# Kernel optimization log

Measured on AMD Instinct MI355X. Metric: run time of the kernel, lower is better.

Reference implementation:

```python
import jax, jax.numpy as jnp
import numpy as np
import math

EMBED_DIM = 1024
N_HEAD = 16
HEAD_DIM = EMBED_DIM // N_HEAD


def setup_inputs() -> dict:
    key = jax.random.key(0)
    ks = jax.random.split(key, 9)
    B, T, C = 4, 2048, EMBED_DIM
    s = 1.0 / math.sqrt(C)
    return {
        "x": jax.random.normal(ks[0], (B, T, C), dtype=jnp.float32),
        "Wq": jax.random.normal(ks[1], (C, C), dtype=jnp.float32) * s,
        "bq": jnp.zeros((C,), dtype=jnp.float32),
        "Wk": jax.random.normal(ks[2], (C, C), dtype=jnp.float32) * s,
        "bk": jnp.zeros((C,), dtype=jnp.float32),
        "Wv": jax.random.normal(ks[3], (C, C), dtype=jnp.float32) * s,
        "bv": jnp.zeros((C,), dtype=jnp.float32),
        "Wp": jax.random.normal(ks[4], (C, C), dtype=jnp.float32) * s,
        "bp": jnp.zeros((C,), dtype=jnp.float32),
    }


def reference(x, Wq, bq, Wk, bk, Wv, bv, Wp, bp):
    B, T, C = x.shape
    H, D = N_HEAD, HEAD_DIM

    def heads(W, b):
        # [B,T,C] -> [B,H,T,D]
        return (x @ W.T + b).reshape(B, T, H, D).transpose(0, 2, 1, 3)

    q = heads(Wq, bq)
    k = heads(Wk, bk)
    v = heads(Wv, bv)

    att = jnp.einsum("bhtd,bhsd->bhts", q, k) * (1.0 / math.sqrt(D))
    causal = jnp.tril(jnp.ones((T, T), dtype=bool))
    att = jnp.where(causal[None, None], att, -jnp.inf)
    att = jax.nn.softmax(att, axis=-1)
    y = jnp.einsum("bhts,bhsd->bhtd", att, v)  # [B,H,T,D]
    y = y.transpose(0, 2, 1, 3).reshape(B, T, C)
    return y @ Wp.T + bp
```

## Files before the change

### kernel.cpp

```cpp
#include <hip/hip_runtime.h>
#include <hip/hip_bf16.h>
#include <cstdint>
#include <cstddef>

#define TQ 2048
#define CDIM 1024
#define NH 16
#define HD 64

typedef __attribute__((ext_vector_type(8))) short bf16x8;
typedef __attribute__((ext_vector_type(4))) float f32x4;
typedef __attribute__((ext_vector_type(16))) float f32x16;

__device__ __forceinline__ unsigned short f2bf(float f) {
  union { float f; unsigned u; } x; x.f = f;
  unsigned r = x.u + 0x7fffu + ((x.u >> 16) & 1u);
  return (unsigned short)(r >> 16);
}

__device__ __forceinline__ unsigned cvtpk(float lo, float hi) {
  unsigned r;
  asm("v_cvt_pk_bf16_f32 %0, %1, %2" : "=v"(r) : "v"(lo), "v"(hi));
  return r;
}

__device__ __forceinline__ void plswap(unsigned& x, unsigned& y) {
  asm("v_permlane32_swap_b32 %0, %1" : "+v"(x), "+v"(y));
}

__device__ __forceinline__ float exp2_fast(float x) {
  float r;
  asm("v_exp_f32 %0, %1" : "=v"(r) : "v"(x));
  return r;
}

__device__ __forceinline__ void gload_lds16(const void* g, void* l) {
  typedef __attribute__((address_space(1))) const void gv;
  typedef __attribute__((address_space(3))) void lv;
  __builtin_amdgcn_global_load_lds((gv*)g, (lv*)l, 16, 0, 0);
}

__global__ void cvt_bf16_kernel(const float* __restrict__ in,
                                unsigned short* __restrict__ out, int n) {
  int stride = gridDim.x * blockDim.x;
  for (int i = blockIdx.x * blockDim.x + threadIdx.x; i * 4 < n; i += stride) {
    float4 v = *(const float4*)(in + (size_t)i * 4);
    ushort4 o;
    o.x = f2bf(v.x); o.y = f2bf(v.y); o.z = f2bf(v.z); o.w = f2bf(v.w);
    *(ushort4*)(out + (size_t)i * 4) = o;
  }
}

__global__ void cvt4_kernel(const float* __restrict__ w0, const float* __restrict__ w1,
                            const float* __restrict__ w2, const float* __restrict__ w3,
                            unsigned short* __restrict__ out) {
  int i = blockIdx.x * blockDim.x + threadIdx.x;
  int which = i >> 18;
  const float* src = which == 0 ? w0 : which == 1 ? w1 : which == 2 ? w2 : w3;
  int off = (i & 262143) * 4;
  float4 v = *(const float4*)(src + off);
  ushort4 o;
  o.x = f2bf(v.x); o.y = f2bf(v.y); o.z = f2bf(v.z); o.w = f2bf(v.w);
  *(ushort4*)(out + (size_t)i * 4) = o;
}

template <int EPI>
__global__ __launch_bounds__(256) void gemm_bt_kernel(
    const unsigned short* __restrict__ A,
    const unsigned short* __restrict__ Bt,
    const float* __restrict__ b0, const float* __restrict__ b1,
    void* __restrict__ outp,
    int M, int N, int K) {
  __shared__ __align__(16) unsigned short As[128 * 64];
  __shared__ __align__(16) unsigned short Bs[128 * 64];

  const int nbm = M >> 7;
  const int nbn = N >> 7;
  const int nwg = nbm * nbn;
  int id = (int)blockIdx.x;
  const int cpx = nwg >> 3;
  id = (id & 7) * cpx + (id >> 3);
  const int tm = id % nbm;
  const int tn = id / nbm;

  const int tid = threadIdx.x;
  const int w = tid >> 6, lane = tid & 63;
  const int g = lane >> 4, c = lane & 15;
  const int wr = w >> 1, wc = w & 1;

  const unsigned short* Ab = A + (size_t)tm * 128 * K;
  const unsigned short* Bb = Bt + (size_t)tn * 128 * K;
  const int Kb = K * 2;

  f32x4 acc[4][4];
#pragma unroll
  for (int i = 0; i < 4; ++i)
#pragma unroll
    for (int j = 0; j < 4; ++j) acc[i][j] = (f32x4){0.f, 0.f, 0.f, 0.f};

  for (int kt = 0; kt < K; kt += 64) {
#pragma unroll
    for (int i = 0; i < 4; ++i) {
      const int seg = w * 4 + i;
      const int off = seg * 1024 + lane * 16;
      const int row = off >> 7;
      const int colB = off & 127;
      gload_lds16((const char*)Ab + (size_t)row * Kb + kt * 2 + colB,
                  (char*)As + seg * 1024);
      gload_lds16((const char*)Bb + (size_t)row * Kb + kt * 2 + colB,
                  (char*)Bs + seg * 1024);
    }
    __syncthreads();
#pragma unroll
    for (int ki = 0; ki < 2; ++ki) {
      bf16x8 af[4], bv[4];
#pragma unroll
      for (int mi = 0; mi < 4; ++mi)
        af[mi] = *(const bf16x8*)(As + (wr * 64 + mi * 16 + c) * 64 + ki * 32 + g * 8);
#pragma unroll
      for (int ni = 0; ni < 4; ++ni)
        bv[ni] = *(const bf16x8*)(Bs + (wc * 64 + ni * 16 + c) * 64 + ki * 32 + g * 8);
#pragma unroll
      for (int mi = 0; mi < 4; ++mi)
#pragma unroll
        for (int ni = 0; ni < 4; ++ni)
          acc[mi][ni] = __builtin_amdgcn_mfma_f32_16x16x32_bf16(
              af[mi], bv[ni], acc[mi][ni], 0, 0, 0);
    }
    __syncthreads();
  }

#pragma unroll
  for (int mi = 0; mi < 4; ++mi) {
#pragma unroll
    for (int ni = 0; ni < 4; ++ni) {
      const int n = tn * 128 + wc * 64 + ni * 16 + c;
#pragma unroll
      for (int e = 0; e < 4; ++e) {
        const int m = tm * 128 + wr * 64 + mi * 16 + g * 4 + e;
        float v = acc[mi][ni][e];
        if (EPI == 1) {
          v += b0[m];
          size_t idx = ((size_t)(n >> 11) * (NH * HD) + m) * TQ + (n & (TQ - 1));
          ((unsigned short*)outp)[idx] = f2bf(v);
        } else if (EPI == 2) {
          v += b0[n];
          ((float*)outp)[(size_t)m * N + n] = v;
        } else {
          unsigned short* O = (unsigned short*)outp;
          if (n < 1024) {
            v += b0[n];
            size_t idx = ((size_t)(m >> 11) * NH + (n >> 6)) * (TQ * HD) +
                         (size_t)(m & (TQ - 1)) * HD + (n & (HD - 1));
            O[idx] = f2bf(v);
          } else {
            int nn = n - 1024;
            v += b1[nn];
            size_t idx = 8388608 + ((size_t)(m >> 11) * NH + (nn >> 6)) * (TQ * HD) +
                         (size_t)(m & (TQ - 1)) * HD + (nn & (HD - 1));
            O[idx] = f2bf(v);
          }
        }
      }
    }
  }
}

__global__ __launch_bounds__(256) void attn_kernel(
    const unsigned short* __restrict__ Q,
    const unsigned short* __restrict__ K,
    const unsigned short* __restrict__ Vt,
    unsigned short* __restrict__ Y) {
  __shared__ __align__(16) unsigned short Ks[2][4096];
  __shared__ __align__(16) unsigned short Vs[2][4096];

  const int tid = (int)threadIdx.x;
  const int w = tid >> 6, lane = tid & 63;
  const int l31 = lane & 31, hi = lane >> 5;
  const int sx = (l31 & 7) << 4;
  const int bh = (int)blockIdx.y;
  const int b = bh >> 4, h = bh & 15;

  const unsigned short* Qb = Q + (size_t)bh * TQ * HD;
  const char* Kb = (const char*)(K + (size_t)bh * TQ * HD);
  const char* Vb = (const char*)(Vt + (size_t)bh * HD * TQ);

  auto stage = [&](int buf, int kt) {
#pragma unroll
    for (int i = 0; i < 2; ++i) {
      const int o = (tid << 4) + (i << 12);
      const int row = o >> 7;
      const int scol = (o & 127) ^ ((row & 7) << 4);
      char* kdst = (char*)&Ks[buf][0] + ((w << 10) + (i << 12));
      char* vdst = (char*)&Vs[buf][0] + ((w << 10) + (i << 12));
      gload_lds16(Kb + (size_t)(kt * 64 + row) * 128 + scol, kdst);
      gload_lds16(Vb + (size_t)row * (TQ * 2) + kt * 128 + scol, vdst);
    }
  };

  const float SC = 0.18033688f;

#pragma unroll 1
  for (int half = 0; half < 2; ++half) {
    const int qt = half ? (15 - (int)blockIdx.x) : (int)blockIdx.x;
    const int q0 = qt * 128 + w * 32;
    const int qg = q0 + l31;
    const int nkv = 2 * qt + 2;

    bf16x8 qf[4];
#pragma unroll
    for (int dk = 0; dk < 4; ++dk)
      qf[dk] = *(const bf16x8*)(Qb + (size_t)qg * HD + dk * 16 + hi * 8);

    f32x16 oac[2];
#pragma unroll
    for (int nb = 0; nb < 2; ++nb)
#pragma unroll
      for (int r = 0; r < 16; ++r) oac[nb][r] = 0.f;
    float mr = -3.0e38f, lr = 0.f;

    stage(0, 0);
    __syncthreads();

    for (int kt = 0; kt < nkv; ++kt) {
      const int cur = kt & 1;
      if (kt + 1 < nkv) stage(cur ^ 1, kt + 1);

      if (kt * 64 <= q0 + 31) {
        const char* Kt = (const char*)&Ks[cur][0];
        const char* Vtile = (const char*)&Vs[cur][0];

        f32x16 s0, s1;
#pragma unroll
        for (int r = 0; r < 16; ++r) { s0[r] = 0.f; s1[r] = 0.f; }
#pragma unroll
        for (int dk = 0; dk < 4; ++dk) {
          bf16x8 kf0 = *(const bf16x8*)(Kt + l31 * 128 + ((dk * 32 + hi * 16) ^ sx));
          bf16x8 kf1 = *(const bf16x8*)(Kt + (32 + l31) * 128 + ((dk * 32 + hi * 16) ^ sx));
          s0 = __builtin_amdgcn_mfma_f32_32x32x16_bf16(kf0, qf[dk], s0, 0, 0, 0);
          s1 = __builtin_amdgcn_mfma_f32_32x32x16_bf16(kf1, qf[dk], s1, 0, 0, 0);
        }

        const bool maskT = (kt * 64 + 63 > q0);
        if (maskT) {
#pragma unroll
          for (int r = 0; r < 16; ++r) {
            int kv0 = kt * 64 + ((r & 3) + 8 * (r >> 2)) + 4 * hi;
            s0[r] = (kv0 <= qg) ? s0[r] * SC : -3.0e38f;
            s1[r] = (kv0 + 32 <= qg) ? s1[r] * SC : -3.0e38f;
          }
        } else {
#pragma unroll
          for (int r = 0; r < 16; ++r) { s0[r] *= SC; s1[r] *= SC; }
        }

        float mt_ = s0[0];
#pragma unroll
        for (int r = 1; r < 16; ++r) mt_ = fmaxf(mt_, s0[r]);
#pragma unroll
        for (int r = 0; r < 16; ++r) mt_ = fmaxf(mt_, s1[r]);
        mt_ = fmaxf(mt_, __shfl_xor(mt_, 32));
        const float mn = fmaxf(mr, mt_);
        const float al = exp2_fast(mr - mn);
        mr = mn;

        float rs = 0.f;
#pragma unroll
        for (int r = 0; r < 16; ++r) { s0[r] = exp2_fast(s0[r] - mn); rs += s0[r]; }
#pragma unroll
        for (int r = 0; r < 16; ++r) { s1[r] = exp2_fast(s1[r] - mn); rs += s1[r]; }
        rs += __shfl_xor(rs, 32);
        lr = lr * al + rs;

#pragma unroll
        for (int nb = 0; nb < 2; ++nb)
#pragma unroll
          for (int r = 0; r < 16; ++r) oac[nb][r] *= al;

        bf16x8 pf[4];
        {
          unsigned a0 = cvtpk(s0[0], s0[1]), b0 = cvtpk(s0[2], s0[3]);
          unsigned c0 = cvtpk(s0[4], s0[5]), d0 = cvtpk(s0[6], s0[7]);
          plswap(a0, c0); plswap(b0, d0);
          unsigned a1 = cvtpk(s0[8], s0[9]), b1 = cvtpk(s0[10], s0[11]);
          unsigned c1 = cvtpk(s0[12], s0[13]), d1 = cvtpk(s0[14], s0[15]);
          plswap(a1, c1); plswap(b1, d1);
          unsigned a2 = cvtpk(s1[0], s1[1]), b2 = cvtpk(s1[2], s1[3]);
          unsigned c2 = cvtpk(s1[4], s1[5]), d2 = cvtpk(s1[6], s1[7]);
          plswap(a2, c2); plswap(b2, d2);
          unsigned a3 = cvtpk(s1[8], s1[9]), b3 = cvtpk(s1[10], s1[11]);
          unsigned c3 = cvtpk(s1[12], s1[13]), d3 = cvtpk(s1[14], s1[15]);
          plswap(a3, c3); plswap(b3, d3);
          union { unsigned u[4]; bf16x8 v; } t;
          t.u[0] = a0; t.u[1] = b0; t.u[2] = c0; t.u[3] = d0; pf[0] = t.v;
          t.u[0] = a1; t.u[1] = b1; t.u[2] = c1; t.u[3] = d1; pf[1] = t.v;
          t.u[0] = a2; t.u[1] = b2; t.u[2] = c2; t.u[3] = d2; pf[2] = t.v;
          t.u[0] = a3; t.u[1] = b3; t.u[2] = c3; t.u[3] = d3; pf[3] = t.v;
        }

#pragma unroll
        for (int nb = 0; nb < 2; ++nb)
#pragma unroll
          for (int ks = 0; ks < 4; ++ks) {
            bf16x8 vf = *(const bf16x8*)(Vtile + (nb * 32 + l31) * 128 +
                                         ((ks * 32 + hi * 16) ^ sx));
            oac[nb] = __builtin_amdgcn_mfma_f32_32x32x16_bf16(vf, pf[ks], oac[nb], 0, 0, 0);
          }
      }
      __syncthreads();
    }

    float inv;
    asm("v_rcp_f32 %0, %1" : "=v"(inv) : "v"(lr));
    unsigned short* Yrow = Y + (size_t)(b * TQ + qg) * CDIM + h * 64;
#pragma unroll
    for (int nb = 0; nb < 2; ++nb)
#pragma unroll
      for (int j = 0; j < 8; ++j) {
        const int dbase = ((2 * j) & 3) + 8 * (j >> 1);
        unsigned lo = f2bf(oac[nb][2 * j] * inv);
        unsigned hi2 = f2bf(oac[nb][2 * j + 1] * inv);
        *(unsigned*)(Yrow + nb * 32 + dbase + 4 * hi) = lo | (hi2 << 16);
      }
  }
}

extern "C" void kernel_launch(void* const* d_in, const int* in_sizes, int n_in,
                              void* d_out, int out_size, void* d_ws, size_t ws_size,
                              hipStream_t stream) {
  (void)in_sizes; (void)n_in; (void)out_size; (void)ws_size;
  const float* x  = (const float*)d_in[0];
  const float* Wq = (const float*)d_in[1];
  const float* bq = (const float*)d_in[2];
  const float* Wk = (const float*)d_in[3];
  const float* bk = (const float*)d_in[4];
  const float* Wv = (const float*)d_in[5];
  const float* bv = (const float*)d_in[6];
  const float* Wp = (const float*)d_in[7];
  const float* bp = (const float*)d_in[8];
  float* out = (float*)d_out;

  char* ws = (char*)d_ws;
  unsigned short* xb  = (unsigned short*)(ws + 0);
  unsigned short* wqb = (unsigned short*)(ws + 16777216);
  unsigned short* wvb = (unsigned short*)(ws + 20971520);
  unsigned short* wpb = (unsigned short*)(ws + 23068672);
  unsigned short* Qh  = (unsigned short*)(ws + 25165824);
  unsigned short* Kh  = (unsigned short*)(ws + 41943040);
  unsigned short* Vt  = (unsigned short*)(ws + 58720256);
  unsigned short* y   = (unsigned short*)(ws + 75497472);

  const int nx = 4 * TQ * CDIM;

  cvt_bf16_kernel<<<4096, 256, 0, stream>>>(x, xb, nx);
  cvt4_kernel<<<4096, 256, 0, stream>>>(Wq, Wk, Wv, Wp, wqb);

  gemm_bt_kernel<4><<<1024, 256, 0, stream>>>(xb, wqb, bq, bk, Qh, 8192, 2048, 1024);
  gemm_bt_kernel<1><<<512, 256, 0, stream>>>(wvb, xb, bv, bv, Vt, 1024, 8192, 1024);

  attn_kernel<<<dim3(8, 64), 256, 0, stream>>>(Qh, Kh, Vt, y);

  gemm_bt_kernel<2><<<512, 256, 0, stream>>>(y, wpb, bp, bp, out, 8192, 1024, 1024);
}
```

Before: 205.6 us.

## Fold softmax scale into Q projection, lazy rescale, fragment-ordered LDS, one tile per block

The softmax scale (with log2e) moves into the Q projection epilogue, which removes the per-score multiply in attention. Online softmax now rescales the output accumulator only when the running max grows by more than a threshold, a conditional-rescale trick. K/V tiles are staged in LDS in MFMA fragment order so each lane reads a contiguous 16 bytes without XOR swizzle. The grid goes from 8 blocks, each doing two paired q-tiles, to 16 blocks with one q-tile each and launch_bounds of 4 waves per EU. The paired-tile load balancing is lost in exchange for more blocks and occupancy, and Q is now rounded to bf16 after scaling.

```diff
diff --git a/kernel.cpp b/kernel.cpp
--- a/kernel.cpp
+++ b/kernel.cpp
@@ -149,7 +149,7 @@
         } else {
           unsigned short* O = (unsigned short*)outp;
           if (n < 1024) {
-            v += b0[n];
+            v = (v + b0[n]) * 0.18033688f;
             size_t idx = ((size_t)(m >> 11) * NH + (n >> 6)) * (TQ * HD) +
                          (size_t)(m & (TQ - 1)) * HD + (n & (HD - 1));
             O[idx] = f2bf(v);
@@ -166,18 +166,17 @@
   }
 }
 
-__global__ __launch_bounds__(256) void attn_kernel(
+__global__ __launch_bounds__(256, 4) void attn_kernel(
     const unsigned short* __restrict__ Q,
     const unsigned short* __restrict__ K,
     const unsigned short* __restrict__ Vt,
     unsigned short* __restrict__ Y) {
-  __shared__ __align__(16) unsigned short Ks[2][4096];
-  __shared__ __align__(16) unsigned short Vs[2][4096];
+  __shared__ __align__(16) char Ks[2][8192];
+  __shared__ __align__(16) char Vs[2][8192];
 
   const int tid = (int)threadIdx.x;
   const int w = tid >> 6, lane = tid & 63;
   const int l31 = lane & 31, hi = lane >> 5;
-  const int sx = (l31 & 7) << 4;
   const int bh = (int)blockIdx.y;
   const int b = bh >> 4, h = bh & 15;
 
@@ -188,141 +187,138 @@
   auto stage = [&](int buf, int kt) {
 #pragma unroll
     for (int i = 0; i < 2; ++i) {
-      const int o = (tid << 4) + (i << 12);
-      const int row = o >> 7;
-      const int scol = (o & 127) ^ ((row & 7) << 4);
-      char* kdst = (char*)&Ks[buf][0] + ((w << 10) + (i << 12));
-      char* vdst = (char*)&Vs[buf][0] + ((w << 10) + (i << 12));
-      gload_lds16(Kb + (size_t)(kt * 64 + row) * 128 + scol, kdst);
-      gload_lds16(Vb + (size_t)row * (TQ * 2) + kt * 128 + scol, vdst);
+      const int s = i * 256 + tid;
+      const int r32 = (s >> 8) * 32 + (s & 31);
+      const int ck = ((s >> 6) & 3) * 32 + ((s >> 5) & 1) * 16;
+      char* kdst = &Ks[buf][0] + i * 4096 + (w << 10);
+      char* vdst = &Vs[buf][0] + i * 4096 + (w << 10);
+      gload_lds16(Kb + (size_t)kt * 8192 + r32 * 128 + ck, kdst);
+      gload_lds16(Vb + (size_t)r32 * 4096 + kt * 128 + ck, vdst);
     }
   };
 
-  const float SC = 0.18033688f;
-
-#pragma unroll 1
-  for (int half = 0; half < 2; ++half) {
-    const int qt = half ? (15 - (int)blockIdx.x) : (int)blockIdx.x;
-    const int q0 = qt * 128 + w * 32;
-    const int qg = q0 + l31;
-    const int nkv = 2 * qt + 2;
-
-    bf16x8 qf[4];
-#pragma unroll
-    for (int dk = 0; dk < 4; ++dk)
-      qf[dk] = *(const bf16x8*)(Qb + (size_t)qg * HD + dk * 16 + hi * 8);
-
-    f32x16 oac[2];
-#pragma unroll
-    for (int nb = 0; nb < 2; ++nb)
-#pragma unroll
-      for (int r = 0; r < 16; ++r) oac[nb][r] = 0.f;
-    float mr = -3.0e38f, lr = 0.f;
-
-    stage(0, 0);
-    __syncthreads();
-
-    for (int kt = 0; kt < nkv; ++kt) {
-      const int cur = kt & 1;
-      if (kt + 1 < nkv) stage(cur ^ 1, kt + 1);
-
-      if (kt * 64 <= q0 + 31) {
-        const char* Kt = (const char*)&Ks[cur][0];
-        const char* Vtile = (const char*)&Vs[cur][0];
-
-        f32x16 s0, s1;
-#pragma unroll
-        for (int r = 0; r < 16; ++r) { s0[r] = 0.f; s1[r] = 0.f; }
-#pragma unroll
-        for (int dk = 0; dk < 4; ++dk) {
-          bf16x8 kf0 = *(const bf16x8*)(Kt + l31 * 128 + ((dk * 32 + hi * 16) ^ sx));
-          bf16x8 kf1 = *(const bf16x8*)(Kt + (32 + l31) * 128 + ((dk * 32 + hi * 16) ^ sx));
-          s0 = __builtin_amdgcn_mfma_f32_32x32x16_bf16(kf0, qf[dk], s0, 0, 0, 0);
-          s1 = __builtin_amdgcn_mfma_f32_32x32x16_bf16(kf1, qf[dk], s1, 0, 0, 0);
+  const int qt = 15 - (int)blockIdx.x;
+  const int q0 = qt * 128 + w * 32;
+  const int qg = q0 + l31;
+  const int nkv = 2 * qt + 2;
+
+  stage(0, 0);
+
+  bf16x8 qf[4];
+#pragma unroll
+  for (int dk = 0; dk < 4; ++dk)
+    qf[dk] = *(const bf16x8*)(Qb + (size_t)qg * HD + dk * 16 + hi * 8);
+
+  f32x16 oac[2];
+#pragma unroll
+  for (int nb = 0; nb < 2; ++nb)
+#pragma unroll
+    for (int r = 0; r < 16; ++r) oac[nb][r] = 0.f;
+  float mr = -3.0e38f, lr = 0.f;
+
+  __syncthreads();
+
+  for (int kt = 0; kt < nkv; ++kt) {
+    const int cur = kt & 1;
+    if (kt + 1 < nkv) stage(cur ^ 1, kt + 1);
+
+    if (kt * 64 <= q0 + 31) {
+      const char* Kt = &Ks[cur][0];
+      const char* Vtile = &Vs[cur][0];
+      const char* Klane = Kt + lane * 16;
+      const char* Vlane = Vtile + lane * 16;
+
+      f32x16 s0, s1;
+#pragma unroll
+      for (int r = 0; r < 16; ++r) { s0[r] = 0.f; s1[r] = 0.f; }
+#pragma unroll
+      for (int dk = 0; dk < 4; ++dk) {
+        bf16x8 kf0 = *(const bf16x8*)(Klane + (dk << 10));
+        bf16x8 kf1 = *(const bf16x8*)(Klane + ((4 + dk) << 10));
+        s0 = __builtin_amdgcn_mfma_f32_32x32x16_bf16(kf0, qf[dk], s0, 0, 0, 0);
+        s1 = __builtin_amdgcn_mfma_f32_32x32x16_bf16(kf1, qf[dk], s1, 0, 0, 0);
+      }
+
+      const bool maskT = (kt * 64 + 63 > q0);
+      if (maskT) {
+#pragma unroll
+        for (int r = 0; r < 16; ++r) {
+          int kv0 = kt * 64 + ((r & 3) + 8 * (r >> 2)) + 4 * hi;
+          s0[r] = (kv0 <= qg) ? s0[r] : -3.0e38f;
+          s1[r] = (kv0 + 32 <= qg) ? s1[r] : -3.0e38f;
         }
-
-        const bool maskT = (kt * 64 + 63 > q0);
-        if (maskT) {
-#pragma unroll
-          for (int r = 0; r < 16; ++r) {
-            int kv0 = kt * 64 + ((r & 3) + 8 * (r >> 2)) + 4 * hi;
-            s0[r] = (kv0 <= qg) ? s0[r] * SC : -3.0e38f;
-            s1[r] = (kv0 + 32 <= qg) ? s1[r] * SC : -3.0e38f;
-          }
-        } else {
-#pragma unroll
-          for (int r = 0; r < 16; ++r) { s0[r] *= SC; s1[r] *= SC; }
-        }
-
-        float mt_ = s0[0];
-#pragma unroll
-        for (int r = 1; r < 16; ++r) mt_ = fmaxf(mt_, s0[r]);
-#pragma unroll
-        for (int r = 0; r < 16; ++r) mt_ = fmaxf(mt_, s1[r]);
-        mt_ = fmaxf(mt_, __shfl_xor(mt_, 32));
+      }
+
+      float mt_ = s0[0];
+#pragma unroll
+      for (int r = 1; r < 16; ++r) mt_ = fmaxf(mt_, s0[r]);
+#pragma unroll
+      for (int r = 0; r < 16; ++r) mt_ = fmaxf(mt_, s1[r]);
+      mt_ = fmaxf(mt_, __shfl_xor(mt_, 32));
+
+      if (!__all(mt_ - mr <= 8.0f)) {
         const float mn = fmaxf(mr, mt_);
         const float al = exp2_fast(mr - mn);
         mr = mn;
-
-        float rs = 0.f;
-#pragma unroll
-        for (int r = 0; r < 16; ++r) { s0[r] = exp2_fast(s0[r] - mn); rs += s0[r]; }
-#pragma unroll
-        for (int r = 0; r < 16; ++r) { s1[r] = exp2_fast(s1[r] - mn); rs += s1[r]; }
-        rs += __shfl_xor(rs, 32);
-        lr = lr * al + rs;
-
+        lr *= al;
 #pragma unroll
         for (int nb = 0; nb < 2; ++nb)
 #pragma unroll
           for (int r = 0; r < 16; ++r) oac[nb][r] *= al;
-
-        bf16x8 pf[4];
-        {
-          unsigned a0 = cvtpk(s0[0], s0[1]), b0 = cvtpk(s0[2], s0[3]);
-          unsigned c0 = cvtpk(s0[4], s0[5]), d0 = cvtpk(s0[6], s0[7]);
-          plswap(a0, c0); plswap(b0, d0);
-          unsigned a1 = cvtpk(s0[8], s0[9]), b1 = cvtpk(s0[10], s0[11]);
-          unsigned c1 = cvtpk(s0[12], s0[13]), d1 = cvtpk(s0[14], s0[15]);
-          plswap(a1, c1); plswap(b1, d1);
-          unsigned a2 = cvtpk(s1[0], s1[1]), b2 = cvtpk(s1[2], s1[3]);
-          unsigned c2 = cvtpk(s1[4], s1[5]), d2 = cvtpk(s1[6], s1[7]);
-          plswap(a2, c2); plswap(b2, d2);
-          unsigned a3 = cvtpk(s1[8], s1[9]), b3 = cvtpk(s1[10], s1[11]);
-          unsigned c3 = cvtpk(s1[12], s1[13]), d3 = cvtpk(s1[14], s1[15]);
-          plswap(a3, c3); plswap(b3, d3);
-          union { unsigned u[4]; bf16x8 v; } t;
-          t.u[0] = a0; t.u[1] = b0; t.u[2] = c0; t.u[3] = d0; pf[0] = t.v;
-          t.u[0] = a1; t.u[1] = b1; t.u[2] = c1; t.u[3] = d1; pf[1] = t.v;
-          t.u[0] = a2; t.u[1] = b2; t.u[2] = c2; t.u[3] = d2; pf[2] = t.v;
-          t.u[0] = a3; t.u[1] = b3; t.u[2] = c3; t.u[3] = d3; pf[3] = t.v;
+      }
+
+      float rs = 0.f;
+#pragma unroll
+      for (int r = 0; r < 16; ++r) { s0[r] = exp2_fast(s0[r] - mr); rs += s0[r]; }
+#pragma unroll
+      for (int r = 0; r < 16; ++r) { s1[r] = exp2_fast(s1[r] - mr); rs += s1[r]; }
+      rs += __shfl_xor(rs, 32);
+      lr += rs;
+
+      bf16x8 pf[4];
+      {
+        unsigned a0 = cvtpk(s0[0], s0[1]), b0 = cvtpk(s0[2], s0[3]);
+        unsigned c0 = cvtpk(s0[4], s0[5]), d0 = cvtpk(s0[6], s0[7]);
+        plswap(a0, c0); plswap(b0, d0);
+        unsigned a1 = cvtpk(s0[8], s0[9]), b1 = cvtpk(s0[10], s0[11]);
+        unsigned c1 = cvtpk(s0[12], s0[13]), d1 = cvtpk(s0[14], s0[15]);
+        plswap(a1, c1); plswap(b1, d1);
+        unsigned a2 = cvtpk(s1[0], s1[1]), b2 = cvtpk(s1[2], s1[3]);
+        unsigned c2 = cvtpk(s1[4], s1[5]), d2 = cvtpk(s1[6], s1[7]);
+        plswap(a2, c2); plswap(b2, d2);
+        unsigned a3 = cvtpk(s1[8], s1[9]), b3 = cvtpk(s1[10], s1[11]);
+        unsigned c3 = cvtpk(s1[12], s1[13]), d3 = cvtpk(s1[14], s1[15]);
+        plswap(a3, c3); plswap(b3, d3);
+        union { unsigned u[4]; bf16x8 v; } t;
+        t.u[0] = a0; t.u[1] = b0; t.u[2] = c0; t.u[3] = d0; pf[0] = t.v;
+        t.u[0] = a1; t.u[1] = b1; t.u[2] = c1; t.u[3] = d1; pf[1] = t.v;
+        t.u[0] = a2; t.u[1] = b2; t.u[2] = c2; t.u[3] = d2; pf[2] = t.v;
+        t.u[0] = a3; t.u[1] = b3; t.u[2] = c3; t.u[3] = d3; pf[3] = t.v;
+      }
+
+#pragma unroll
+      for (int nb = 0; nb < 2; ++nb)
+#pragma unroll
+        for (int ks = 0; ks < 4; ++ks) {
+          bf16x8 vf = *(const bf16x8*)(Vlane + (((nb << 2) + ks) << 10));
+          oac[nb] = __builtin_amdgcn_mfma_f32_32x32x16_bf16(vf, pf[ks], oac[nb], 0, 0, 0);
         }
-
-#pragma unroll
-        for (int nb = 0; nb < 2; ++nb)
-#pragma unroll
-          for (int ks = 0; ks < 4; ++ks) {
-            bf16x8 vf = *(const bf16x8*)(Vtile + (nb * 32 + l31) * 128 +
-                                         ((ks * 32 + hi * 16) ^ sx));
-            oac[nb] = __builtin_amdgcn_mfma_f32_32x32x16_bf16(vf, pf[ks], oac[nb], 0, 0, 0);
-          }
-      }
-      __syncthreads();
-    }
-
-    float inv;
-    asm("v_rcp_f32 %0, %1" : "=v"(inv) : "v"(lr));
-    unsigned short* Yrow = Y + (size_t)(b * TQ + qg) * CDIM + h * 64;
-#pragma unroll
-    for (int nb = 0; nb < 2; ++nb)
-#pragma unroll
-      for (int j = 0; j < 8; ++j) {
-        const int dbase = ((2 * j) & 3) + 8 * (j >> 1);
-        unsigned lo = f2bf(oac[nb][2 * j] * inv);
-        unsigned hi2 = f2bf(oac[nb][2 * j + 1] * inv);
-        *(unsigned*)(Yrow + nb * 32 + dbase + 4 * hi) = lo | (hi2 << 16);
-      }
+    }
+    __syncthreads();
   }
+
+  float inv;
+  asm("v_rcp_f32 %0, %1" : "=v"(inv) : "v"(lr));
+  unsigned short* Yrow = Y + (size_t)(b * TQ + qg) * CDIM + h * 64;
+#pragma unroll
+  for (int nb = 0; nb < 2; ++nb)
+#pragma unroll
+    for (int j = 0; j < 8; ++j) {
+      const int dbase = ((2 * j) & 3) + 8 * (j >> 1);
+      unsigned lo = f2bf(oac[nb][2 * j] * inv);
+      unsigned hi2 = f2bf(oac[nb][2 * j + 1] * inv);
+      *(unsigned*)(Yrow + nb * 32 + dbase + 4 * hi) = lo | (hi2 << 16);
+    }
 }
 
 extern "C" void kernel_launch(void* const* d_in, const int* in_sizes, int n_in,
@@ -358,7 +354,7 @@
   gemm_bt_kernel<4><<<1024, 256, 0, stream>>>(xb, wqb, bq, bk, Qh, 8192, 2048, 1024);
   gemm_bt_kernel<1><<<512, 256, 0, stream>>>(wvb, xb, bv, bv, Vt, 1024, 8192, 1024);
 
-  attn_kernel<<<dim3(8, 64), 256, 0, stream>>>(Qh, Kh, Vt, y);
+  attn_kernel<<<dim3(16, 64), 256, 0, stream>>>(Qh, Kh, Vt, y);
 
   gemm_bt_kernel<2><<<512, 256, 0, stream>>>(y, wpb, bp, bp, out, 8192, 1024, 1024);
 }
```

After: 245.7 us. 1.19x slower.
